# Optimization experiments

Hardware: AMD Instinct MI355X
Metric: run time of the kernel (lower is better)

The kernel has to match this reference:

```python
import jax, jax.numpy as jnp
import numpy as np

EPS = 1e-08


def setup_inputs() -> dict:
    key = jax.random.key(0)
    k1, k2 = jax.random.split(key)
    z = jax.random.normal(k1, (64, 768, 32, 32), dtype=jnp.float32)
    memory = jax.random.normal(k2, (100, 768), dtype=jnp.float32)
    return {"z": z, "memory": memory}


def _l2norm(x, axis=-1):
    # matches F.normalize(dim=-1): x / max(||x||, 1e-12)
    n = jnp.sqrt(jnp.sum(x * x, axis=axis, keepdims=True))
    return x / jnp.maximum(n, 1e-12)


def reference(z, memory):
    B, C, H, W = z.shape
    M = memory.shape[0]
    # (B,C,H,W) -> (B, N, C) with N = H*W
    z_flat = jnp.transpose(z, (0, 2, 3, 1)).reshape(B, H * W, C)
    z_norm = _l2norm(z_flat)
    mem_norm = _l2norm(memory)
    scores = jnp.einsum('bnc,mc->bnm', z_norm, mem_norm)  # (B, N, M)
    w = jax.nn.softmax(scores, axis=-1)
    lam = 1.0 / M
    d = w - lam
    attn_w = jax.nn.relu(d) * w / (jnp.abs(d) + EPS)      # hard shrinkage
    attn_w = attn_w / (jnp.sum(attn_w, axis=-1, keepdims=True) + EPS)
    z_hat_flat = jnp.einsum('bnm,mc->bnc', attn_w, memory)
    z_hat = jnp.transpose(z_hat_flat.reshape(B, H, W, C), (0, 3, 1, 2))
    return (z_hat, attn_w)
```

## Files before the change

### kernel.cpp

```cpp
#include <hip/hip_runtime.h>

#define EPSF 1e-8f

typedef __fp16   h2v   __attribute__((ext_vector_type(2)));
typedef _Float16 half8 __attribute__((ext_vector_type(8)));
typedef float    f32x16 __attribute__((ext_vector_type(16)));

constexpr int Bn = 64, Cc = 768, Nn = 1024, Mm = 100;

__device__ inline f32x16 zero16() {
    f32x16 z;
#pragma unroll
    for (int i = 0; i < 16; ++i) z[i] = 0.f;
    return z;
}

union U4H8 { uint4 u; half8 h; h2v p[4]; };

__device__ inline unsigned pkr(float a, float b) {
    union { h2v p; unsigned u; } cv;
    cv.p = __builtin_amdgcn_cvt_pkrtz(a, b);
    return cv.u;
}

__device__ inline void gload_lds16(const void* g, void* s) {
    __builtin_amdgcn_global_load_lds(
        (const __attribute__((address_space(1))) unsigned int*)g,
        (__attribute__((address_space(3))) unsigned int*)s, 16, 0, 0);
}

__global__ __launch_bounds__(256) void prep_kernel(const float* __restrict__ mem,
                                                   _Float16* __restrict__ mhiF,
                                                   _Float16* __restrict__ mloF,
                                                   _Float16* __restrict__ muF) {
    int m = blockIdx.x, t = threadIdx.x;
    float inv = 0.f;
    if (m < Mm) {
        float ss = 0.f;
        for (int c = t; c < Cc; c += 256) { float v = mem[m * Cc + c]; ss += v * v; }
        __shared__ float red[256];
        red[t] = ss; __syncthreads();
        for (int s = 128; s > 0; s >>= 1) { if (t < s) red[t] += red[t + s]; __syncthreads(); }
        inv = 1.f / fmaxf(sqrtf(red[0]), 1e-12f);
    }
    for (int c = t; c < Cc; c += 256) {
        float v = (m < Mm) ? mem[m * Cc + c] : 0.f;
        float nv = v * inv;
        _Float16 hh = (_Float16)nv;
        _Float16 ll = (_Float16)(nv - (float)hh);
        int cs = c >> 4, hb = (c >> 3) & 1, j = c & 7, mt = m >> 5, ml = m & 31;
        size_t idx = ((size_t)(cs * 4 + mt) * 64 + hb * 32 + ml) * 8 + j;
        mhiF[idx] = hh;
        mloF[idx] = ll;
        int ct = c >> 5, cl = c & 31, ms = m >> 4, hm = (m >> 3) & 1, jm = m & 7;
        size_t idx2 = ((size_t)(ct * 8 + ms) * 64 + hm * 32 + cl) * 8 + jm;
        muF[idx2] = (_Float16)v;
    }
}

__global__ __launch_bounds__(256) void score_kernel(
    const float* __restrict__ z, const _Float16* __restrict__ mhiF,
    const _Float16* __restrict__ mloF, float* __restrict__ attn_out) {
    __shared__ uint4 fbuf[2][4][2][256];

    const int tid = threadIdx.x;
    const int w = tid >> 6;
    const int l = tid & 63;
    const int wid = (blockIdx.x << 2) | w;
    const int b = wid >> 5;
    const int pxb = (wid & 31) * 32;
    const int pl = l & 31;
    const int h = l >> 5;
    const float* zr = z + (size_t)b * Cc * Nn + pxb + pl + (size_t)h * 8 * Nn;
    const uint4* mh4 = (const uint4*)mhiF;
    const uint4* ml4 = (const uint4*)mloF;
    const uint4* gh = mh4 + w * 64 + l;
    const uint4* gl = ml4 + w * 64 + l;

    f32x16 acc[4] = {zero16(), zero16(), zero16(), zero16()};
    float ss = 0.f;
    float zbufA[4][8], zbufB[4][8];

#pragma unroll
    for (int i = 0; i < 4; ++i) {
        gload_lds16(gh + i * 256, &fbuf[0][i][0][w * 64]);
        gload_lds16(gl + i * 256, &fbuf[0][i][1][w * 64]);
    }
#pragma unroll
    for (int i = 0; i < 4; ++i)
#pragma unroll
        for (int j = 0; j < 8; ++j)
            zbufA[i][j] = __builtin_nontemporal_load(&zr[(size_t)(i * 16 + j) * Nn]);
    __builtin_amdgcn_sched_barrier(0);
    asm volatile("s_waitcnt vmcnt(32)" ::: "memory");
    __builtin_amdgcn_sched_barrier(0);
    __builtin_amdgcn_s_barrier();
    __builtin_amdgcn_sched_barrier(0);

    auto round_body = [&](int RR, float (&ZC)[4][8], float (&ZN)[4][8], int FB) {
        const bool more = (RR + 1 < 12);
        if (more) {
#pragma unroll
            for (int i = 0; i < 4; ++i) {
                gload_lds16(gh + ((RR + 1) * 4 + i) * 256, &fbuf[FB ^ 1][i][0][w * 64]);
                gload_lds16(gl + ((RR + 1) * 4 + i) * 256, &fbuf[FB ^ 1][i][1][w * 64]);
            }
#pragma unroll
            for (int i = 0; i < 4; ++i)
#pragma unroll
                for (int j = 0; j < 8; ++j)
                    ZN[i][j] = __builtin_nontemporal_load(
                        &zr[(size_t)(((RR + 1) * 4 + i) * 16 + j) * Nn]);
        }
#pragma unroll
        for (int i = 0; i < 4; ++i) {
            U4H8 zh, zl8;
#pragma unroll
            for (int t = 0; t < 4; ++t) {
                float u = ZC[i][2 * t], v = ZC[i][2 * t + 1];
                h2v p = __builtin_amdgcn_cvt_pkrtz(u, v);
                zh.p[t] = p;
                zl8.p[t] = __builtin_amdgcn_cvt_pkrtz(u - (float)p.x, v - (float)p.y);
                ss += u * u + v * v;
            }
            U4H8 ah, al;
#pragma unroll
            for (int mt = 0; mt < 4; ++mt) {
                ah.u = fbuf[FB][i][0][mt * 64 + l];
                al.u = fbuf[FB][i][1][mt * 64 + l];
                acc[mt] = __builtin_amdgcn_mfma_f32_32x32x16_f16(ah.h, zh.h, acc[mt], 0, 0, 0);
                acc[mt] = __builtin_amdgcn_mfma_f32_32x32x16_f16(al.h, zh.h, acc[mt], 0, 0, 0);
                acc[mt] = __builtin_amdgcn_mfma_f32_32x32x16_f16(ah.h, zl8.h, acc[mt], 0, 0, 0);
            }
        }
        if (more) {
            __builtin_amdgcn_sched_barrier(0);
            asm volatile("s_waitcnt vmcnt(32)" ::: "memory");
            __builtin_amdgcn_sched_barrier(0);
            __builtin_amdgcn_s_barrier();
            __builtin_amdgcn_sched_barrier(0);
        }
    };

#pragma unroll 1
    for (int rp = 0; rp < 6; ++rp) {
        round_body(2 * rp, zbufA, zbufB, 0);
        round_body(2 * rp + 1, zbufB, zbufA, 1);
    }

    ss += __shfl_xor(ss, 32);
    float invn = 1.f / fmaxf(sqrtf(ss), 1e-12f);

    float a_[64];
#pragma unroll
    for (int r = 0; r < 64; ++r) {
        int mt = r >> 4, rr = r & 15;
        float v = acc[mt][rr] * invn;
        if (r >= 52) v = -3.0e38f;
        else if (r >= 48) v = (h == 0) ? v : -3.0e38f;
        a_[r] = v;
    }
    float mx = -3.0e38f;
#pragma unroll
    for (int r = 0; r < 52; ++r) mx = fmaxf(mx, a_[r]);
    mx = fmaxf(mx, __shfl_xor(mx, 32));

    float sum = 0.f;
#pragma unroll
    for (int r = 0; r < 52; ++r) { float e = expf(a_[r] - mx); a_[r] = e; sum += e; }
    sum += __shfl_xor(sum, 32);
    float itot = 1.f / sum;

    float asum = 0.f;
#pragma unroll
    for (int r = 0; r < 52; ++r) {
        float w_ = a_[r] * itot;
        float d = w_ - 0.01f;
        float aa = (d > 0.f) ? (d * w_) / (d + EPSF) : 0.f;
        a_[r] = aa; asum += aa;
    }
    asum += __shfl_xor(asum, 32);
    float ia = 1.f / (asum + EPSF);
#pragma unroll
    for (int r = 0; r < 52; ++r) a_[r] *= ia;

    {
        size_t ob = (size_t)(wid * 32 + pl) * (size_t)Mm;
#pragma unroll
        for (int g = 0; g < 13; ++g) {
            int r0 = g * 4;
            int m0 = (r0 >> 4) * 32 + 8 * ((r0 >> 2) & 3) + 4 * h;
            if (g < 12 || h == 0) {
                float4 v = make_float4(a_[r0], a_[r0 + 1], a_[r0 + 2], a_[r0 + 3]);
                *(float4*)&attn_out[ob + m0] = v;
            }
        }
    }
}

__global__ __launch_bounds__(256, 4) void recon_kernel(
    const _Float16* __restrict__ muF, const float* __restrict__ attn_out,
    float* __restrict__ zhat) {
    const int tid = threadIdx.x;
    const int w = tid >> 6;
    const int l = tid & 63;
    const int gb = blockIdx.x;
    const int b = gb >> 5;
    const int pxb = (gb & 31) * 32;
    const int pl = l & 31;
    const int h = l >> 5;

    const float* ap = attn_out + (size_t)(gb * 32 + pl) * (size_t)Mm;
    uint4 bfr[8];
#pragma unroll
    for (int ms = 0; ms < 6; ++ms) {
        float4 fa = *(const float4*)&ap[ms * 16 + h * 8];
        float4 fb = *(const float4*)&ap[ms * 16 + h * 8 + 4];
        bfr[ms] = make_uint4(pkr(fa.x, fa.y), pkr(fa.z, fa.w),
                             pkr(fb.x, fb.y), pkr(fb.z, fb.w));
    }
    {
        float4 fa = (h == 0) ? *(const float4*)&ap[96] : make_float4(0.f, 0.f, 0.f, 0.f);
        bfr[6] = make_uint4(pkr(fa.x, fa.y), pkr(fa.z, fa.w), 0u, 0u);
        bfr[7] = make_uint4(0u, 0u, 0u, 0u);
    }

    const uint4* mu4 = (const uint4*)muF;
    float* zo = zhat + (size_t)b * Cc * Nn + pxb + pl;
    const int ct0 = w * 6;
#pragma unroll 1
    for (int cti = 0; cti < 6; cti += 2) {
        int ct = ct0 + cti;
        f32x16 a2 = zero16(), a3 = zero16();
#pragma unroll
        for (int ms = 0; ms < 7; ++ms) {
            U4H8 A0, A1, Bf;
            A0.u = mu4[(ct * 8 + ms) * 64 + l];
            A1.u = mu4[((ct + 1) * 8 + ms) * 64 + l];
            Bf.u = bfr[ms];
            a2 = __builtin_amdgcn_mfma_f32_32x32x16_f16(A0.h, Bf.h, a2, 0, 0, 0);
            a3 = __builtin_amdgcn_mfma_f32_32x32x16_f16(A1.h, Bf.h, a3, 0, 0, 0);
        }
#pragma unroll
        for (int r = 0; r < 16; ++r) {
            int cl = (r & 3) + 8 * (r >> 2) + 4 * h;
            __builtin_nontemporal_store(a2[r], &zo[(size_t)(ct * 32 + cl) * Nn]);
            __builtin_nontemporal_store(a3[r], &zo[(size_t)(ct * 32 + 32 + cl) * Nn]);
        }
    }
}

extern "C" void kernel_launch(void* const* d_in, const int* in_sizes, int n_in,
                              void* d_out, int out_size, void* d_ws, size_t ws_size,
                              hipStream_t stream) {
    const float* z = (const float*)d_in[0];
    const float* mem = (const float*)d_in[1];
    float* out = (float*)d_out;
    float* zhat = out;
    float* attn = out + (size_t)Bn * Cc * Nn;
    _Float16* mhiF = (_Float16*)d_ws;
    _Float16* mloF = mhiF + 48 * 4 * 64 * 8;
    _Float16* muF = mloF + 48 * 4 * 64 * 8;

    prep_kernel<<<128, 256, 0, stream>>>(mem, mhiF, mloF, muF);
    score_kernel<<<512, 256, 0, stream>>>(z, mhiF, mloF, attn);
    recon_kernel<<<2048, 256, 0, stream>>>(muF, attn, zhat);
}
```

Measured before the change: 112.2 us.

## Switch score kernel to 16x16x32 MFMA tiles padding memory to 112

Moves the score GEMM from 32x32x16 MFMA tiles, which padded the 100 memory rows up to 128, to 16x16x32 tiles that pad only to 112. This cuts the wasted MFMA work. Each wave now handles 16 pixels, and blocks grow to 512 threads with 8 waves. The waves share loading of a single interleaved hi/lo memory buffer into LDS, with uneven slot counts per wave. Softmax reductions gain an extra shuffle stage, and the larger blocks may change occupancy and register pressure.

```diff
diff --git a/kernel.cpp b/kernel.cpp
--- a/kernel.cpp
+++ b/kernel.cpp
@@ -4,10 +4,12 @@
 
 typedef __fp16   h2v   __attribute__((ext_vector_type(2)));
 typedef _Float16 half8 __attribute__((ext_vector_type(8)));
+typedef float    f32x4  __attribute__((ext_vector_type(4)));
 typedef float    f32x16 __attribute__((ext_vector_type(16)));
 
 constexpr int Bn = 64, Cc = 768, Nn = 1024, Mm = 100;
 
+__device__ inline f32x4 zero4() { f32x4 z; z[0]=z[1]=z[2]=z[3]=0.f; return z; }
 __device__ inline f32x16 zero16() {
     f32x16 z;
 #pragma unroll
@@ -30,8 +32,7 @@
 }
 
 __global__ __launch_bounds__(256) void prep_kernel(const float* __restrict__ mem,
-                                                   _Float16* __restrict__ mhiF,
-                                                   _Float16* __restrict__ mloF,
+                                                   _Float16* __restrict__ mF,
                                                    _Float16* __restrict__ muF) {
     int m = blockIdx.x, t = threadIdx.x;
     float inv = 0.f;
@@ -48,94 +49,94 @@
         float nv = v * inv;
         _Float16 hh = (_Float16)nv;
         _Float16 ll = (_Float16)(nv - (float)hh);
-        int cs = c >> 4, hb = (c >> 3) & 1, j = c & 7, mt = m >> 5, ml = m & 31;
-        size_t idx = ((size_t)(cs * 4 + mt) * 64 + hb * 32 + ml) * 8 + j;
-        mhiF[idx] = hh;
-        mloF[idx] = ll;
+        if (m < 112) {
+            int s = c >> 5, kg = (c >> 3) & 3, j = c & 7, tt = m >> 4, ml = m & 15;
+            size_t g = (size_t)(s * 7 + tt) * 2;
+            mF[((g + 0) * 64 + kg * 16 + ml) * 8 + j] = hh;
+            mF[((g + 1) * 64 + kg * 16 + ml) * 8 + j] = ll;
+        }
         int ct = c >> 5, cl = c & 31, ms = m >> 4, hm = (m >> 3) & 1, jm = m & 7;
-        size_t idx2 = ((size_t)(ct * 8 + ms) * 64 + hm * 32 + cl) * 8 + jm;
-        muF[idx2] = (_Float16)v;
-    }
-}
-
-__global__ __launch_bounds__(256) void score_kernel(
-    const float* __restrict__ z, const _Float16* __restrict__ mhiF,
-    const _Float16* __restrict__ mloF, float* __restrict__ attn_out) {
-    __shared__ uint4 fbuf[2][4][2][256];
+        muF[((size_t)(ct * 8 + ms) * 64 + hm * 32 + cl) * 8 + jm] = (_Float16)v;
+    }
+}
+
+__global__ __launch_bounds__(512, 4) void score_kernel(
+    const float* __restrict__ z, const _Float16* __restrict__ mF,
+    float* __restrict__ attn_out) {
+    __shared__ uint4 fbuf[2][28][64];
 
     const int tid = threadIdx.x;
     const int w = tid >> 6;
     const int l = tid & 63;
-    const int wid = (blockIdx.x << 2) | w;
-    const int b = wid >> 5;
-    const int pxb = (wid & 31) * 32;
-    const int pl = l & 31;
-    const int h = l >> 5;
-    const float* zr = z + (size_t)b * Cc * Nn + pxb + pl + (size_t)h * 8 * Nn;
-    const uint4* mh4 = (const uint4*)mhiF;
-    const uint4* ml4 = (const uint4*)mloF;
-    const uint4* gh = mh4 + w * 64 + l;
-    const uint4* gl = ml4 + w * 64 + l;
-
-    f32x16 acc[4] = {zero16(), zero16(), zero16(), zero16()};
+    const int wid = (blockIdx.x << 3) | w;
+    const int b = wid >> 6;
+    const int pxb = (wid & 63) * 16;
+    const int px = l & 15;
+    const int kg = l >> 4;
+    const float* zr = z + (size_t)b * Cc * Nn + pxb + px + (size_t)kg * 8 * Nn;
+    const uint4* mf4 = (const uint4*)mF;
+    const int nslot = (w < 4) ? 4 : 3;
+    const int q0 = (w < 4) ? (w * 4) : (16 + (w - 4) * 3);
+
+    f32x4 acc[7];
+#pragma unroll
+    for (int t = 0; t < 7; ++t) acc[t] = zero4();
     float ss = 0.f;
-    float zbufA[4][8], zbufB[4][8];
-
-#pragma unroll
-    for (int i = 0; i < 4; ++i) {
-        gload_lds16(gh + i * 256, &fbuf[0][i][0][w * 64]);
-        gload_lds16(gl + i * 256, &fbuf[0][i][1][w * 64]);
-    }
+    float zA[2][8], zB[2][8];
+
 #pragma unroll
     for (int i = 0; i < 4; ++i)
+        if (i < nslot) gload_lds16(mf4 + (size_t)(q0 + i) * 64 + l, &fbuf[0][q0 + i][0]);
+#pragma unroll
+    for (int p = 0; p < 2; ++p)
 #pragma unroll
         for (int j = 0; j < 8; ++j)
-            zbufA[i][j] = __builtin_nontemporal_load(&zr[(size_t)(i * 16 + j) * Nn]);
+            zA[p][j] = __builtin_nontemporal_load(&zr[(size_t)(p * 32 + j) * Nn]);
     __builtin_amdgcn_sched_barrier(0);
-    asm volatile("s_waitcnt vmcnt(32)" ::: "memory");
+    asm volatile("s_waitcnt vmcnt(16)" ::: "memory");
     __builtin_amdgcn_sched_barrier(0);
     __builtin_amdgcn_s_barrier();
     __builtin_amdgcn_sched_barrier(0);
 
-    auto round_body = [&](int RR, float (&ZC)[4][8], float (&ZN)[4][8], int FB) {
+    auto round_body = [&](int RR, float (&ZC)[2][8], float (&ZN)[2][8], int FB) {
         const bool more = (RR + 1 < 12);
         if (more) {
 #pragma unroll
-            for (int i = 0; i < 4; ++i) {
-                gload_lds16(gh + ((RR + 1) * 4 + i) * 256, &fbuf[FB ^ 1][i][0][w * 64]);
-                gload_lds16(gl + ((RR + 1) * 4 + i) * 256, &fbuf[FB ^ 1][i][1][w * 64]);
-            }
-#pragma unroll
             for (int i = 0; i < 4; ++i)
+                if (i < nslot)
+                    gload_lds16(mf4 + ((size_t)(RR + 1) * 28 + q0 + i) * 64 + l,
+                                &fbuf[FB ^ 1][q0 + i][0]);
+#pragma unroll
+            for (int p = 0; p < 2; ++p)
 #pragma unroll
                 for (int j = 0; j < 8; ++j)
-                    ZN[i][j] = __builtin_nontemporal_load(
-                        &zr[(size_t)(((RR + 1) * 4 + i) * 16 + j) * Nn]);
-        }
-#pragma unroll
-        for (int i = 0; i < 4; ++i) {
+                    ZN[p][j] = __builtin_nontemporal_load(
+                        &zr[(size_t)(((RR + 1) * 2 + p) * 32 + j) * Nn]);
+        }
+#pragma unroll
+        for (int p = 0; p < 2; ++p) {
             U4H8 zh, zl8;
 #pragma unroll
             for (int t = 0; t < 4; ++t) {
-                float u = ZC[i][2 * t], v = ZC[i][2 * t + 1];
-                h2v p = __builtin_amdgcn_cvt_pkrtz(u, v);
-                zh.p[t] = p;
-                zl8.p[t] = __builtin_amdgcn_cvt_pkrtz(u - (float)p.x, v - (float)p.y);
+                float u = ZC[p][2 * t], v = ZC[p][2 * t + 1];
+                h2v q = __builtin_amdgcn_cvt_pkrtz(u, v);
+                zh.p[t] = q;
+                zl8.p[t] = __builtin_amdgcn_cvt_pkrtz(u - (float)q.x, v - (float)q.y);
                 ss += u * u + v * v;
             }
-            U4H8 ah, al;
-#pragma unroll
-            for (int mt = 0; mt < 4; ++mt) {
-                ah.u = fbuf[FB][i][0][mt * 64 + l];
-                al.u = fbuf[FB][i][1][mt * 64 + l];
-                acc[mt] = __builtin_amdgcn_mfma_f32_32x32x16_f16(ah.h, zh.h, acc[mt], 0, 0, 0);
-                acc[mt] = __builtin_amdgcn_mfma_f32_32x32x16_f16(al.h, zh.h, acc[mt], 0, 0, 0);
-                acc[mt] = __builtin_amdgcn_mfma_f32_32x32x16_f16(ah.h, zl8.h, acc[mt], 0, 0, 0);
+#pragma unroll
+            for (int t = 0; t < 7; ++t) {
+                U4H8 ah, al;
+                ah.u = fbuf[FB][p * 14 + t * 2][l];
+                al.u = fbuf[FB][p * 14 + t * 2 + 1][l];
+                acc[t] = __builtin_amdgcn_mfma_f32_16x16x32_f16(ah.h, zh.h, acc[t], 0, 0, 0);
+                acc[t] = __builtin_amdgcn_mfma_f32_16x16x32_f16(al.h, zh.h, acc[t], 0, 0, 0);
+                acc[t] = __builtin_amdgcn_mfma_f32_16x16x32_f16(ah.h, zl8.h, acc[t], 0, 0, 0);
             }
         }
         if (more) {
             __builtin_amdgcn_sched_barrier(0);
-            asm volatile("s_waitcnt vmcnt(32)" ::: "memory");
+            asm volatile("s_waitcnt vmcnt(16)" ::: "memory");
             __builtin_amdgcn_sched_barrier(0);
             __builtin_amdgcn_s_barrier();
             __builtin_amdgcn_sched_barrier(0);
@@ -144,54 +145,57 @@
 
 #pragma unroll 1
     for (int rp = 0; rp < 6; ++rp) {
-        round_body(2 * rp, zbufA, zbufB, 0);
-        round_body(2 * rp + 1, zbufB, zbufA, 1);
-    }
-
+        round_body(2 * rp, zA, zB, 0);
+        round_body(2 * rp + 1, zB, zA, 1);
+    }
+
+    ss += __shfl_xor(ss, 16);
     ss += __shfl_xor(ss, 32);
     float invn = 1.f / fmaxf(sqrtf(ss), 1e-12f);
 
-    float a_[64];
-#pragma unroll
-    for (int r = 0; r < 64; ++r) {
-        int mt = r >> 4, rr = r & 15;
-        float v = acc[mt][rr] * invn;
-        if (r >= 52) v = -3.0e38f;
-        else if (r >= 48) v = (h == 0) ? v : -3.0e38f;
-        a_[r] = v;
-    }
+    float a_[28];
+#pragma unroll
+    for (int t = 0; t < 7; ++t)
+#pragma unroll
+        for (int rr = 0; rr < 4; ++rr) {
+            float v = acc[t][rr] * invn;
+            if (t == 6 && kg != 0) v = -3.0e38f;
+            a_[t * 4 + rr] = v;
+        }
     float mx = -3.0e38f;
 #pragma unroll
-    for (int r = 0; r < 52; ++r) mx = fmaxf(mx, a_[r]);
+    for (int r = 0; r < 28; ++r) mx = fmaxf(mx, a_[r]);
+    mx = fmaxf(mx, __shfl_xor(mx, 16));
     mx = fmaxf(mx, __shfl_xor(mx, 32));
 
     float sum = 0.f;
 #pragma unroll
-    for (int r = 0; r < 52; ++r) { float e = expf(a_[r] - mx); a_[r] = e; sum += e; }
+    for (int r = 0; r < 28; ++r) { float e = expf(a_[r] - mx); a_[r] = e; sum += e; }
+    sum += __shfl_xor(sum, 16);
     sum += __shfl_xor(sum, 32);
     float itot = 1.f / sum;
 
     float asum = 0.f;
 #pragma unroll
-    for (int r = 0; r < 52; ++r) {
+    for (int r = 0; r < 28; ++r) {
         float w_ = a_[r] * itot;
         float d = w_ - 0.01f;
         float aa = (d > 0.f) ? (d * w_) / (d + EPSF) : 0.f;
         a_[r] = aa; asum += aa;
     }
+    asum += __shfl_xor(asum, 16);
     asum += __shfl_xor(asum, 32);
     float ia = 1.f / (asum + EPSF);
 #pragma unroll
-    for (int r = 0; r < 52; ++r) a_[r] *= ia;
+    for (int r = 0; r < 28; ++r) a_[r] *= ia;
 
     {
-        size_t ob = (size_t)(wid * 32 + pl) * (size_t)Mm;
-#pragma unroll
-        for (int g = 0; g < 13; ++g) {
-            int r0 = g * 4;
-            int m0 = (r0 >> 4) * 32 + 8 * ((r0 >> 2) & 3) + 4 * h;
-            if (g < 12 || h == 0) {
-                float4 v = make_float4(a_[r0], a_[r0 + 1], a_[r0 + 2], a_[r0 + 3]);
+        size_t ob = (size_t)(wid * 16 + px) * (size_t)Mm;
+#pragma unroll
+        for (int t = 0; t < 7; ++t) {
+            if (t < 6 || kg == 0) {
+                int m0 = 16 * t + 4 * kg;
+                float4 v = make_float4(a_[4 * t], a_[4 * t + 1], a_[4 * t + 2], a_[4 * t + 3]);
                 *(float4*)&attn_out[ob + m0] = v;
             }
         }
@@ -258,11 +262,10 @@
     float* out = (float*)d_out;
     float* zhat = out;
     float* attn = out + (size_t)Bn * Cc * Nn;
-    _Float16* mhiF = (_Float16*)d_ws;
-    _Float16* mloF = mhiF + 48 * 4 * 64 * 8;
-    _Float16* muF = mloF + 48 * 4 * 64 * 8;
-
-    prep_kernel<<<128, 256, 0, stream>>>(mem, mhiF, mloF, muF);
-    score_kernel<<<512, 256, 0, stream>>>(z, mhiF, mloF, attn);
+    _Float16* mF = (_Float16*)d_ws;
+    _Float16* muF = mF + 24 * 7 * 2 * 64 * 8;
+
+    prep_kernel<<<128, 256, 0, stream>>>(mem, mF, muF);
+    score_kernel<<<512, 512, 0, stream>>>(z, mF, attn);
     recon_kernel<<<2048, 256, 0, stream>>>(muF, attn, zhat);
 }
```

Result: slower. 115.4 us (+2.8%).
